# Performance work log

Measured on AMD Instinct MI355X. Metric: run time of the kernel, lower is better.

Reference implementation:

```python
import jax, jax.numpy as jnp
import numpy as np

# Precompute flat gather indices replicating matA's banded structure.
# Row (layer l, offset i) of matA sums d[i : i+l], for l in 1..255, i in 0..255-l.
# Equivalently diff = cumsum_pad[i+l] - cumsum_pad[i].
def _build_indices():
    lo, hi, lid = [], [], []
    for l in range(1, 256):
        n = 256 - l
        i = np.arange(n)
        lo.append(i)
        hi.append(i + l)
        lid.append(np.full(n, l - 1))
    return (np.concatenate(lo), np.concatenate(hi), np.concatenate(lid))

_IDX_LO, _IDX_HI, _LAYER_ID = _build_indices()  # each length 32640
IDX_LO = jnp.asarray(_IDX_LO)
IDX_HI = jnp.asarray(_IDX_HI)
LAYER_ID = jnp.asarray(_LAYER_ID)
# elements averaged per layer: B * (256 - l)
_COUNTS = (256 - np.arange(1, 256)).astype(np.float32)
COUNTS = jnp.asarray(_COUNTS)


def setup_inputs() -> dict:
    key = jax.random.key(0)
    k1, k2, k3 = jax.random.split(key, 3)
    B = 512
    d1layer = jax.random.normal(k1, (B, 1, 255), dtype=jnp.float32)
    hvec = jax.random.normal(k2, (B, 32640), dtype=jnp.float32)
    mask = jax.random.uniform(k3, (B, 255), dtype=jnp.float32)
    return {"d1layer": d1layer, "hvec": hvec, "mask": mask}


def reference(d1layer, hvec, mask):
    B = d1layer.shape[0]
    m = jnp.power(mask, 2.5)  # [B, 255]
    d = d1layer[:, 0, :]  # [B, 255]
    # padded cumulative sum: c[:, k] = sum_{j<k} d[:, j], shape [B, 256]
    c = jnp.concatenate(
        [jnp.zeros((B, 1), dtype=d.dtype), jnp.cumsum(d, axis=1)], axis=1
    )
    # banded windowed sums for all 32640 (layer, offset) pairs at once
    matAd = c[:, IDX_HI] - c[:, IDX_LO]  # [B, 32640]
    w = m[:, LAYER_ID]  # [B, 32640], mask[:, layer-1] broadcast over offsets
    sq = jnp.square(matAd - hvec) * w  # [B, 32640]
    per_layer_sum = jax.ops.segment_sum(
        jnp.sum(sq, axis=0), LAYER_ID, num_segments=255
    )  # [255]
    loss_layers = per_layer_sum / (COUNTS * jnp.float32(B))  # per-layer mean
    return jnp.mean(loss_layers)
```

## Files before the change

kernel.cpp:

```cpp
#include <hip/hip_runtime.h>

#define NLAYER 255
#define SEQ    256
#define TOTJ   32640
#define PG     4
#define PASSES_PER_GROUP 32
#define THREADS 256

__global__ __launch_bounds__(THREADS) void main_kernel(
        const float* __restrict__ d1layer,
        const float* __restrict__ hvec,
        const float* __restrict__ mask,
        float* __restrict__ partials)
{
    __shared__ float c[SEQ];
    __shared__ float w[SEQ];
    __shared__ float wsum[THREADS / 64];
    __shared__ float red[THREADS / 64];

    const int g = blockIdx.x;
    const int b = blockIdx.y;
    const int t = threadIdx.x;
    const int lane = t & 63;
    const int wid  = t >> 6;

    if (t < NLAYER) {
        float mk = mask[b * NLAYER + t];
        w[t + 1] = mk * mk * sqrtf(mk) / (float)(NLAYER - t);
    }

    float v = (t > 0) ? d1layer[b * NLAYER + (t - 1)] : 0.0f;
    #pragma unroll
    for (int off = 1; off < 64; off <<= 1) {
        float u = __shfl_up(v, off, 64);
        if (lane >= off) v += u;
    }
    if (lane == 63) wsum[wid] = v;
    __syncthreads();
    float woff = 0.0f;
    #pragma unroll
    for (int i = 0; i < THREADS / 64; ++i)
        if (i < wid) woff += wsum[i];
    c[t] = v + woff;
    __syncthreads();

    const float* hrow = hvec + (size_t)b * TOTJ;
    const int p0 = g * PASSES_PER_GROUP + 1;

    float acc = 0.0f;
    #pragma unroll 4
    for (int pp = 0; pp < PASSES_PER_GROUP; ++pp) {
        const int p  = p0 + pp;
        const int n  = 256 - p;
        const int m1 = p - 1;
        const int S1 = 256 * m1 - ((m1 * (m1 + 1)) >> 1);
        const int m2 = 256 - p;
        const int S2 = 256 * m2 - ((m2 * (m2 + 1)) >> 1);

        if (t < NLAYER) {
            const bool first = t < n;
            const int layer = first ? p : (257 - p);
            const int i     = first ? t : (t - n);
            const int hidx  = first ? (S1 + t) : (S2 + t - n);
            float h  = hrow[hidx];
            float dd = (c[i + layer] - c[i]) - h;
            acc += dd * dd * w[layer];
        }
    }

    #pragma unroll
    for (int off = 32; off > 0; off >>= 1)
        acc += __shfl_down(acc, off, 64);
    if (lane == 0) red[wid] = acc;
    __syncthreads();
    if (t == 0) {
        float s = 0.0f;
        #pragma unroll
        for (int i = 0; i < THREADS / 64; ++i) s += red[i];
        partials[b * PG + g] = s;
    }
}

__global__ __launch_bounds__(256) void reduce_kernel(
        const float* __restrict__ partials, int n, int B,
        float* __restrict__ out)
{
    __shared__ float red[4];
    float acc = 0.0f;
    for (int i = threadIdx.x; i < n; i += 256) acc += partials[i];
    #pragma unroll
    for (int off = 32; off > 0; off >>= 1)
        acc += __shfl_down(acc, off, 64);
    int lane = threadIdx.x & 63, wid = threadIdx.x >> 6;
    if (lane == 0) red[wid] = acc;
    __syncthreads();
    if (threadIdx.x == 0) {
        float s = 0.0f;
        #pragma unroll
        for (int i = 0; i < 4; ++i) s += red[i];
        out[0] = s / ((float)NLAYER * (float)B);
    }
}

extern "C" void kernel_launch(void* const* d_in, const int* in_sizes, int n_in,
                              void* d_out, int out_size, void* d_ws, size_t ws_size,
                              hipStream_t stream) {
    const float* d1layer = (const float*)d_in[0];
    const float* hvec    = (const float*)d_in[1];
    const float* mask    = (const float*)d_in[2];
    float* out = (float*)d_out;

    const int B = in_sizes[2] / NLAYER;

    float* partials = (float*)d_ws;

    dim3 grid(PG, B);
    main_kernel<<<grid, THREADS, 0, stream>>>(d1layer, hvec, mask, partials);
    reduce_kernel<<<1, 256, 0, stream>>>(partials, PG * B, B, out);
}
```

Before: 112.2 us.

## Use constexpr packed index table with float4 loads of hvec

The per-pass index arithmetic is replaced by a compile-time device table that packs the layer, low and high shared-memory byte offsets for each flattened element. hvec and the table are read as float4/uint4 in linear chunks, and the cumsum array in shared memory is padded to reduce bank conflicts. The intent is to make global loads wide and coalesced. The cost is an extra 128KB table read from global memory on every call, which adds memory traffic and relies on caching.

```diff
diff --git a/kernel.cpp b/kernel.cpp
--- a/kernel.cpp
+++ b/kernel.cpp
@@ -3,9 +3,27 @@
 #define NLAYER 255
 #define SEQ    256
 #define TOTJ   32640
-#define PG     4
-#define PASSES_PER_GROUP 32
+#define CHUNKS 4
+#define CHUNK_J (TOTJ / CHUNKS)
+#define CHUNK_F4 (CHUNK_J / 4)
 #define THREADS 256
+
+struct TblT { unsigned int v[TOTJ]; };
+static constexpr TblT make_tbl() {
+    TblT t{};
+    int idx = 0;
+    for (int l = 1; l <= NLAYER; ++l) {
+        for (int i = 0; i < 256 - l; ++i) {
+            unsigned int lid4 = (unsigned int)((l - 1) * 4);
+            unsigned int s0   = (unsigned int)((i + (i >> 3)) * 4);
+            int hi = i + l;
+            unsigned int s1   = (unsigned int)((hi + (hi >> 3)) * 4);
+            t.v[idx++] = lid4 | (s0 << 10) | (s1 << 21);
+        }
+    }
+    return t;
+}
+__device__ constexpr TblT TBL = make_tbl();
 
 __global__ __launch_bounds__(THREADS) void main_kernel(
         const float* __restrict__ d1layer,
@@ -13,20 +31,20 @@
         const float* __restrict__ mask,
         float* __restrict__ partials)
 {
-    __shared__ float c[SEQ];
-    __shared__ float w[SEQ];
+    __shared__ float cs[288];
+    __shared__ float w[NLAYER];
     __shared__ float wsum[THREADS / 64];
     __shared__ float red[THREADS / 64];
 
-    const int g = blockIdx.x;
-    const int b = blockIdx.y;
-    const int t = threadIdx.x;
-    const int lane = t & 63;
-    const int wid  = t >> 6;
+    const int chunk = blockIdx.x;
+    const int b     = blockIdx.y;
+    const int t     = threadIdx.x;
+    const int lane  = t & 63;
+    const int wid   = t >> 6;
 
     if (t < NLAYER) {
         float mk = mask[b * NLAYER + t];
-        w[t + 1] = mk * mk * sqrtf(mk) / (float)(NLAYER - t);
+        w[t] = mk * mk * sqrtf(mk) / (float)(NLAYER - t);
     }
 
     float v = (t > 0) ? d1layer[b * NLAYER + (t - 1)] : 0.0f;
@@ -41,31 +59,35 @@
     #pragma unroll
     for (int i = 0; i < THREADS / 64; ++i)
         if (i < wid) woff += wsum[i];
-    c[t] = v + woff;
+    cs[t + (t >> 3)] = v + woff;
     __syncthreads();
 
-    const float* hrow = hvec + (size_t)b * TOTJ;
-    const int p0 = g * PASSES_PER_GROUP + 1;
+    const float4* hv4 = (const float4*)(hvec + (size_t)b * TOTJ + chunk * CHUNK_J);
+    const uint4*  tb4 = (const uint4*)(TBL.v + chunk * CHUNK_J);
+    const char* csb = (const char*)cs;
+    const char* wb  = (const char*)w;
 
     float acc = 0.0f;
     #pragma unroll 4
-    for (int pp = 0; pp < PASSES_PER_GROUP; ++pp) {
-        const int p  = p0 + pp;
-        const int n  = 256 - p;
-        const int m1 = p - 1;
-        const int S1 = 256 * m1 - ((m1 * (m1 + 1)) >> 1);
-        const int m2 = 256 - p;
-        const int S2 = 256 * m2 - ((m2 * (m2 + 1)) >> 1);
+    for (int f4 = t; f4 < CHUNK_F4; f4 += THREADS) {
+        float4 h  = hv4[f4];
+        uint4  tv = tb4[f4];
 
-        if (t < NLAYER) {
-            const bool first = t < n;
-            const int layer = first ? p : (257 - p);
-            const int i     = first ? t : (t - n);
-            const int hidx  = first ? (S1 + t) : (S2 + t - n);
-            float h  = hrow[hidx];
-            float dd = (c[i + layer] - c[i]) - h;
-            acc += dd * dd * w[layer];
-        }
+        unsigned int e0 = tv.x, e1 = tv.y, e2 = tv.z, e3 = tv.w;
+
+        float d0 = (*(const float*)(csb + (e0 >> 21)) -
+                    *(const float*)(csb + ((e0 >> 10) & 0x7FF))) - h.x;
+        float d1 = (*(const float*)(csb + (e1 >> 21)) -
+                    *(const float*)(csb + ((e1 >> 10) & 0x7FF))) - h.y;
+        float d2 = (*(const float*)(csb + (e2 >> 21)) -
+                    *(const float*)(csb + ((e2 >> 10) & 0x7FF))) - h.z;
+        float d3 = (*(const float*)(csb + (e3 >> 21)) -
+                    *(const float*)(csb + ((e3 >> 10) & 0x7FF))) - h.w;
+
+        acc += d0 * d0 * *(const float*)(wb + (e0 & 0x3FF));
+        acc += d1 * d1 * *(const float*)(wb + (e1 & 0x3FF));
+        acc += d2 * d2 * *(const float*)(wb + (e2 & 0x3FF));
+        acc += d3 * d3 * *(const float*)(wb + (e3 & 0x3FF));
     }
 
     #pragma unroll
@@ -77,7 +99,7 @@
         float s = 0.0f;
         #pragma unroll
         for (int i = 0; i < THREADS / 64; ++i) s += red[i];
-        partials[b * PG + g] = s;
+        partials[b * CHUNKS + chunk] = s;
     }
 }
 
@@ -114,7 +136,7 @@
 
     float* partials = (float*)d_ws;
 
-    dim3 grid(PG, B);
+    dim3 grid(CHUNKS, B);
     main_kernel<<<grid, THREADS, 0, stream>>>(d1layer, hvec, mask, partials);
-    reduce_kernel<<<1, 256, 0, stream>>>(partials, PG * B, B, out);
+    reduce_kernel<<<1, 256, 0, stream>>>(partials, CHUNKS * B, B, out);
 }
```

New measurement: 105.2 us. 6.3% less time.
